# Kernel tuning notes

Measured on AMD Instinct MI355X. Metric: run time of the kernel, lower is better.

## Reference

```python
import jax, jax.numpy as jnp
import numpy as np

N = 40000          # nodes
E = 1280000        # edges (avg degree 32)
S = 64             # num_scalars
V = 16             # num_vectors
R = 32             # num_radial
CUTOFF = 10.0


def setup_inputs() -> dict:
    key = jax.random.key(0)
    ks = jax.random.split(key, 12)
    scalars = jax.random.normal(ks[0], (N, S), dtype=jnp.float32)
    vectors = jax.random.normal(ks[1], (N, V, 3), dtype=jnp.float32)
    edge_index = jax.random.randint(ks[2], (2, E), 0, N, dtype=jnp.int64)
    edge_vec = jax.random.normal(ks[3], (E, 3), dtype=jnp.float32)
    # radial_net: Linear(R,R) -> SiLU -> Linear(R, S + 2V)
    W1 = jax.random.normal(ks[4], (R, R), dtype=jnp.float32) * 0.1
    b1 = jnp.zeros((R,), dtype=jnp.float32)
    W2 = jax.random.normal(ks[5], (R, S + 2 * V), dtype=jnp.float32) * 0.1
    b2 = jnp.zeros((S + 2 * V,), dtype=jnp.float32)
    # attention: Linear(2S+R, S) -> SiLU -> Linear(S, 1)
    Wa1 = jax.random.normal(ks[6], (2 * S + R, S), dtype=jnp.float32) * 0.1
    ba1 = jnp.zeros((S,), dtype=jnp.float32)
    Wa2 = jax.random.normal(ks[7], (S, 1), dtype=jnp.float32) * 0.1
    ba2 = jnp.zeros((1,), dtype=jnp.float32)
    return dict(scalars=scalars, vectors=vectors, edge_vec=edge_vec,
                W1=W1, b1=b1, W2=W2, b2=b2,
                Wa1=Wa1, ba1=ba1, Wa2=Wa2, ba2=ba2,
                edge_index=edge_index)


def reference(scalars, vectors, edge_vec, W1, b1, W2, b2, Wa1, ba1, Wa2, ba2, edge_index):
    src = edge_index[0]  # j (source)
    dst = edge_index[1]  # i (target / aggregation index)

    d = jnp.linalg.norm(edge_vec, axis=-1)                 # [E]
    d_safe = jnp.clip(d[:, None], 1e-8, None)              # [E,1]

    # Bessel radial basis with cosine cutoff
    freqs = (jnp.arange(1, R + 1, dtype=jnp.float32) * np.pi / CUTOFF)
    bessel = jnp.sin(freqs * d[:, None]) / d_safe          # [E,R]
    cut = 0.5 * (jnp.cos(np.pi * d[:, None] / CUTOFF) + 1.0)
    cut = cut * (d[:, None] < CUTOFF).astype(jnp.float32)
    rbf = bessel * cut                                     # [E,R]

    # spherical harmonics (lmax=1); vector already normalized, sh = [1, y, z, x]
    unit = edge_vec / d_safe                               # [E,3]
    sh_weight = jnp.stack([unit[:, 1], unit[:, 2], unit[:, 0]], axis=-1)  # [E,3]

    # radial filter MLP
    filters = jax.nn.silu(rbf @ W1 + b1) @ W2 + b2         # [E, S+2V]
    scalar_filter = filters[:, :S]
    vector_filter = filters[:, S:S + V]
    vector_gate = filters[:, S + V:]

    s_i = scalars[dst]                                     # [E,S]
    s_j = scalars[src]                                     # [E,S]
    v_j = vectors[src]                                     # [E,V,3]

    scalar_message = s_j * scalar_filter                   # [E,S]
    vector_message = (v_j * vector_filter[:, :, None]
                      + vector_gate[:, :, None] * sh_weight[:, None, :])  # [E,V,3]

    att_in = jnp.concatenate([s_i, s_j, rbf], axis=-1)     # [E, 2S+R]
    att = jax.nn.sigmoid(jax.nn.silu(att_in @ Wa1 + ba1) @ Wa2 + ba2)  # [E,1]

    scalar_message = att * scalar_message
    vector_message = att[:, :, None] * vector_message

    scalar_aggr = jax.ops.segment_sum(scalar_message, dst, num_segments=N)
    vector_aggr = jax.ops.segment_sum(vector_message, dst, num_segments=N)

    return scalars + scalar_aggr, vectors + vector_aggr
```

## Files before the change

kernel.cpp:

```cpp
#include <hip/hip_runtime.h>

static constexpr int N_ = 40000;
static constexpr int E_ = 1280000;
static constexpr int NS = N_ * 64;
static constexpr int NV = N_ * 48;

typedef _Float16 half2_t __attribute__((ext_vector_type(2)));
typedef _Float16 half8_t __attribute__((ext_vector_type(8)));
typedef float float4_t __attribute__((ext_vector_type(4)));
typedef unsigned int uint;

__device__ __forceinline__ float silu_f(float x) { return __fdividef(x, 1.f + __expf(-x)); }
__device__ __forceinline__ int rfl(int x) { return __builtin_amdgcn_readfirstlane(x); }

static constexpr int PATT_BLOCKS = 512;
__global__ __launch_bounds__(256) void k_patt(
    const float* __restrict__ scalars, const float* __restrict__ Wa1,
    const float* __restrict__ ba1,
    _Float16* __restrict__ P1h, _Float16* __restrict__ P2h)
{
    int gw   = (blockIdx.x * 256 + threadIdx.x) >> 6;
    int lane = threadIdx.x & 63;
    float w[128];
#pragma unroll
    for (int k = 0; k < 128; k++) w[k] = Wa1[k * 64 + lane];
    float bias = ba1[lane];
    for (int n = gw; n < N_; n += PATT_BLOCKS * 4) {
        float sv = scalars[(size_t)n * 64 + lane];
        float a1 = bias, a2 = 0.f;
#pragma unroll
        for (int k = 0; k < 64; k++) {
            float sk = __shfl(sv, k, 64);
            a1 = fmaf(sk, w[k], a1);
            a2 = fmaf(sk, w[64 + k], a2);
        }
        P1h[(size_t)n * 64 + lane] = (_Float16)a1;
        P2h[(size_t)n * 64 + lane] = (_Float16)a2;
    }
}

__global__ void k_convp(const float* __restrict__ scalars, const float* __restrict__ vectors,
                        _Float16* __restrict__ sc16p, _Float16* __restrict__ vec16p)
{
    int t = blockIdx.x * 256 + threadIdx.x;
    if (t < N_ * 16) {
        int n = t >> 4, bl = t & 15;
        const float* srow = scalars + (size_t)n * 64;
        half2_t a, b;
        a.x = (_Float16)srow[bl];
        a.y = (_Float16)srow[16 + bl];
        b.x = (_Float16)srow[32 + bl];
        b.y = (_Float16)srow[48 + bl];
        uint2 u; u.x = __builtin_bit_cast(uint, a); u.y = __builtin_bit_cast(uint, b);
        *(uint2*)(sc16p + (size_t)n * 64 + bl * 4) = u;
    } else {
        int tt = t - N_ * 16;
        int n = tt >> 4, bl = tt & 15;
        const float* vrow = vectors + (size_t)n * 48 + bl * 3;
        half2_t a, b;
        a.x = (_Float16)vrow[0];
        a.y = (_Float16)vrow[1];
        b.x = (_Float16)vrow[2];
        b.y = (_Float16)0.f;
        uint2 u; u.x = __builtin_bit_cast(uint, a); u.y = __builtin_bit_cast(uint, b);
        *(uint2*)(vec16p + (size_t)n * 64 + bl * 4) = u;
    }
}

__global__ void k_pack(const float* __restrict__ W1, const float* __restrict__ Wa1,
                       const float* __restrict__ W2, uint* __restrict__ tbl,
                       uint* __restrict__ tbl2)
{
    int t = blockIdx.x * 256 + threadIdx.x;
    if (t < 1536) {
        int j = t >> 4, q = t & 15;
        int k0 = 2 * q, k1 = 2 * q + 1;
        float a = (j < 64) ? Wa1[(128 + k0) * 64 + j] : W1[k0 * 32 + (j - 64)];
        float b = (j < 64) ? Wa1[(128 + k1) * 64 + j] : W1[k1 * 32 + (j - 64)];
        half2_t v; v.x = (_Float16)a; v.y = (_Float16)b;
        tbl[t] = __builtin_bit_cast(uint, v);
    } else if (t < 3072) {
        int tt = t - 1536;
        int j = tt >> 4, q = tt & 15;
        half2_t v;
        v.x = (_Float16)W2[(2 * q + 0) * 96 + j];
        v.y = (_Float16)W2[(2 * q + 1) * 96 + j];
        tbl2[tt] = __builtin_bit_cast(uint, v);
    }
}

__global__ void k_rank(const int* __restrict__ eidx, int* __restrict__ cnt,
                       int* __restrict__ r)
{
    int e = blockIdx.x * 256 + threadIdx.x;
    r[e] = atomicAdd(&cnt[eidx[E_ + e]], 1);
}

__global__ void k_scan1(const int* __restrict__ cnt, int* __restrict__ row_start,
                        int* __restrict__ bsum)
{
    __shared__ int buf[1024];
    int b = blockIdx.x, tid = threadIdx.x;
    int idx = b * 1024 + tid;
    int v = (idx < N_) ? cnt[idx] : 0;
    buf[tid] = v;
    __syncthreads();
    for (int off = 1; off < 1024; off <<= 1) {
        int t = (tid >= off) ? buf[tid - off] : 0;
        __syncthreads();
        buf[tid] += t;
        __syncthreads();
    }
    if (idx < N_) row_start[idx] = buf[tid] - v;
    if (tid == 1023) bsum[b] = buf[1023];
}

__global__ void k_scan2(const int* __restrict__ bsum, int* __restrict__ boff)
{
    if (threadIdx.x == 0) {
        int s = 0;
        for (int b = 0; b < 40; b++) { boff[b] = s; s += bsum[b]; }
    }
}

__global__ void k_scan3(const int* __restrict__ boff, int* __restrict__ row_start)
{
    int idx = blockIdx.x * 1024 + threadIdx.x;
    if (idx < N_) row_start[idx] += boff[blockIdx.x];
    if (idx == N_) row_start[N_] = E_;
}

__global__ void k_place(const int* __restrict__ eidx, const int* __restrict__ row_start,
                        const int* __restrict__ r, int* __restrict__ perm)
{
    int e = blockIdx.x * 256 + threadIdx.x;
    int dst = eidx[E_ + e];
    perm[row_start[dst] + r[e]] = e;
}

__global__ __launch_bounds__(256, 3) void k_edges_sorted(
    const float* __restrict__ edge_vec, const int* __restrict__ eidx,
    const int* __restrict__ perm,
    const _Float16* __restrict__ P1h, const _Float16* __restrict__ P2h,
    const uint* __restrict__ tbl, const float* __restrict__ b1,
    const float* __restrict__ Wa2, const float* __restrict__ ba2,
    float4* __restrict__ attsh, int* __restrict__ srcbuf, uint* __restrict__ hbufp)
{
    __shared__ char lds_raw[4 * 12544];
    int tid = threadIdx.x;
    int wid = tid >> 6, lane = tid & 63;
    char* wbase = lds_raw + wid * 12544;
    int bl = lane & 15, bq = lane >> 4;

    int i = blockIdx.x * 256 + tid;
    int e = perm[i];
    int src = eidx[e];
    int dst = eidx[E_ + e];

    float ev0 = edge_vec[3 * e + 0];
    float ev1 = edge_vec[3 * e + 1];
    float ev2 = edge_vec[3 * e + 2];
    float d = sqrtf(fmaf(ev0, ev0, fmaf(ev1, ev1, ev2 * ev2)));
    float inv_d = __fdividef(1.f, fmaxf(d, 1e-8f));
    float cut = (d < 10.f) ? 0.5f * (__cosf(0.31415927f * d) + 1.f) : 0.f;
    float cutd = cut * inv_d;
    float sh0 = ev1 * inv_d, sh1 = ev2 * inv_d, sh2 = ev0 * inv_d;

    float th = 0.31415927f * d;
    float scur = __sinf(th);
    float twoC = 2.f * __cosf(th);
    float sprev = 0.f;
    uint rbf2[16];
#pragma unroll
    for (int q = 0; q < 16; q++) {
        float r0 = scur * cutd;
        float snext = fmaf(twoC, scur, -sprev);
        sprev = scur; scur = snext;
        float r1 = scur * cutd;
        snext = fmaf(twoC, scur, -sprev);
        sprev = scur; scur = snext;
        half2_t v; v.x = (_Float16)r0; v.y = (_Float16)r1;
        rbf2[q] = __builtin_bit_cast(uint, v);
    }
    {
        uint4* rw = (uint4*)(wbase + lane * 64);
        rw[0] = make_uint4(rbf2[0], rbf2[1], rbf2[2], rbf2[3]);
        rw[1] = make_uint4(rbf2[4], rbf2[5], rbf2[6], rbf2[7]);
        rw[2] = make_uint4(rbf2[8], rbf2[9], rbf2[10], rbf2[11]);
        rw[3] = make_uint4(rbf2[12], rbf2[13], rbf2[14], rbf2[15]);
    }
    uint4 bfr[6];
#pragma unroll
    for (int u = 0; u < 6; u++)
        bfr[u] = *(const uint4*)(tbl + (u * 16 + bl) * 16 + bq * 4);

    uint4 afr[4];
#pragma unroll
    for (int t = 0; t < 4; t++)
        afr[t] = *(const uint4*)(wbase + (t * 16 + bl) * 64 + bq * 16);

    _Float16* gtile = (_Float16*)wbase;
#pragma unroll
    for (int t = 0; t < 4; t++) {
        half8_t av = __builtin_bit_cast(half8_t, afr[t]);
        int eb = t * 16 + bq * 4;
#pragma unroll
        for (int u = 0; u < 6; u++) {
            float4_t dd = __builtin_amdgcn_mfma_f32_16x16x32_f16(
                av, __builtin_bit_cast(half8_t, bfr[u]), (float4_t)(0.f), 0, 0, 0);
            int col = u * 16 + bl;
            gtile[(eb + 0) * 98 + col] = (_Float16)dd[0];
            gtile[(eb + 1) * 98 + col] = (_Float16)dd[1];
            gtile[(eb + 2) * 98 + col] = (_Float16)dd[2];
            gtile[(eb + 3) * 98 + col] = (_Float16)dd[3];
        }
    }
    const uint* grow = (const uint*)(wbase + (size_t)lane * 196);

    const uint2* p1h = (const uint2*)(P1h + (size_t)dst * 64);
    const uint2* p2h = (const uint2*)(P2h + (size_t)src * 64);
    float logit = ba2[0];
#pragma unroll
    for (int q = 0; q < 16; q++) {
        uint2 ua = p1h[q];
        uint2 ub = p2h[q];
        half2_t s01 = __builtin_bit_cast(half2_t, ua.x) + __builtin_bit_cast(half2_t, ub.x)
                    + __builtin_bit_cast(half2_t, grow[2 * q + 0]);
        half2_t s23 = __builtin_bit_cast(half2_t, ua.y) + __builtin_bit_cast(half2_t, ub.y)
                    + __builtin_bit_cast(half2_t, grow[2 * q + 1]);
        logit = fmaf(silu_f((float)s01.x), Wa2[4 * q + 0], logit);
        logit = fmaf(silu_f((float)s01.y), Wa2[4 * q + 1], logit);
        logit = fmaf(silu_f((float)s23.x), Wa2[4 * q + 2], logit);
        logit = fmaf(silu_f((float)s23.y), Wa2[4 * q + 3], logit);
    }
    float att = __fdividef(1.f, 1.f + __expf(-logit));

    uint hp[16];
#pragma unroll
    for (int q = 0; q < 16; q++) {
        half2_t gg = __builtin_bit_cast(half2_t, grow[32 + q]);
        half2_t v;
        v.x = (_Float16)silu_f((float)gg.x + b1[2 * q + 0]);
        v.y = (_Float16)silu_f((float)gg.y + b1[2 * q + 1]);
        hp[q] = __builtin_bit_cast(uint, v);
    }
    uint4* hrow4 = (uint4*)(hbufp + (size_t)i * 16);
#pragma unroll
    for (int q = 0; q < 4; q++)
        hrow4[q] = make_uint4(hp[4 * q + 0], hp[4 * q + 1], hp[4 * q + 2], hp[4 * q + 3]);
    attsh[i] = make_float4(att, sh0, sh1, sh2);
    srcbuf[i] = src;
}

__global__ __launch_bounds__(256, 4) void k_gather_mfma(
    const float* __restrict__ scalars, const float* __restrict__ vectors,
    const _Float16* __restrict__ sc16p, const _Float16* __restrict__ vec16p,
    const float* __restrict__ b2,
    const int* __restrict__ row_start,
    const float4* __restrict__ attsh, const int* __restrict__ srcbuf,
    const uint* __restrict__ hbuf, const uint* __restrict__ tbl2,
    float* __restrict__ out)
{
    int wid  = threadIdx.x >> 6;
    int lane = threadIdx.x & 63;
    int n    = blockIdx.x * 4 + wid;
    int bl = lane & 15, bq = lane >> 4;
    int rs = rfl(row_start[n]);
    int re = rfl(row_start[n + 1]);

    uint4 bfr2[6];
#pragma unroll
    for (int u = 0; u < 6; u++)
        bfr2[u] = *(const uint4*)(tbl2 + (u * 16 + bl) * 16 + bq * 4);

    float b2s[4];
#pragma unroll
    for (int u = 0; u < 4; u++) b2s[u] = b2[u * 16 + bl];
    float bvf = b2[64 + bl], bvg = b2[80 + bl];

    float accS0 = 0.f, accS1 = 0.f, accS2 = 0.f, accS3 = 0.f;
    float accV0 = 0.f, accV1 = 0.f, accV2 = 0.f;

    for (int i0 = rs; i0 < re; i0 += 16) {
        uint4 av4 = make_uint4(0u, 0u, 0u, 0u);
        if (i0 + bl < re)
            av4 = *(const uint4*)(hbuf + (size_t)(i0 + bl) * 16 + bq * 4);
        half8_t av = __builtin_bit_cast(half8_t, av4);

        float4_t d0 = __builtin_amdgcn_mfma_f32_16x16x32_f16(av, __builtin_bit_cast(half8_t, bfr2[0]), (float4_t)(0.f), 0, 0, 0);
        float4_t d1 = __builtin_amdgcn_mfma_f32_16x16x32_f16(av, __builtin_bit_cast(half8_t, bfr2[1]), (float4_t)(0.f), 0, 0, 0);
        float4_t d2 = __builtin_amdgcn_mfma_f32_16x16x32_f16(av, __builtin_bit_cast(half8_t, bfr2[2]), (float4_t)(0.f), 0, 0, 0);
        float4_t d3 = __builtin_amdgcn_mfma_f32_16x16x32_f16(av, __builtin_bit_cast(half8_t, bfr2[3]), (float4_t)(0.f), 0, 0, 0);
        float4_t d4 = __builtin_amdgcn_mfma_f32_16x16x32_f16(av, __builtin_bit_cast(half8_t, bfr2[4]), (float4_t)(0.f), 0, 0, 0);
        float4_t d5 = __builtin_amdgcn_mfma_f32_16x16x32_f16(av, __builtin_bit_cast(half8_t, bfr2[5]), (float4_t)(0.f), 0, 0, 0);

#pragma unroll
        for (int r = 0; r < 4; r++) {
            int slot = i0 + bq * 4 + r;
            int ok = (slot < re);
            int cs = ok ? slot : (re - 1);
            float4 as = attsh[cs];
            float att = ok ? as.x : 0.f;
            int src = srcbuf[cs];
            uint2 su = *(const uint2*)(sc16p + (size_t)src * 64 + bl * 4);
            uint2 vu = *(const uint2*)(vec16p + (size_t)src * 64 + bl * 4);
            half2_t s01 = __builtin_bit_cast(half2_t, su.x);
            half2_t s23 = __builtin_bit_cast(half2_t, su.y);
            half2_t v01 = __builtin_bit_cast(half2_t, vu.x);
            half2_t v23 = __builtin_bit_cast(half2_t, vu.y);
            accS0 = fmaf(att * (float)s01.x, d0[r] + b2s[0], accS0);
            accS1 = fmaf(att * (float)s01.y, d1[r] + b2s[1], accS1);
            accS2 = fmaf(att * (float)s23.x, d2[r] + b2s[2], accS2);
            accS3 = fmaf(att * (float)s23.y, d3[r] + b2s[3], accS3);
            float vf = d4[r] + bvf;
            float vg = d5[r] + bvg;
            accV0 = fmaf(att, fmaf((float)v01.x, vf, vg * as.y), accV0);
            accV1 = fmaf(att, fmaf((float)v01.y, vf, vg * as.z), accV1);
            accV2 = fmaf(att, fmaf((float)v23.x, vf, vg * as.w), accV2);
        }
    }

    accS0 += __shfl_xor(accS0, 16, 64); accS0 += __shfl_xor(accS0, 32, 64);
    accS1 += __shfl_xor(accS1, 16, 64); accS1 += __shfl_xor(accS1, 32, 64);
    accS2 += __shfl_xor(accS2, 16, 64); accS2 += __shfl_xor(accS2, 32, 64);
    accS3 += __shfl_xor(accS3, 16, 64); accS3 += __shfl_xor(accS3, 32, 64);
    accV0 += __shfl_xor(accV0, 16, 64); accV0 += __shfl_xor(accV0, 32, 64);
    accV1 += __shfl_xor(accV1, 16, 64); accV1 += __shfl_xor(accV1, 32, 64);
    accV2 += __shfl_xor(accV2, 16, 64); accV2 += __shfl_xor(accV2, 32, 64);

    if (bq == 0) {
        size_t o = (size_t)n * 64 + bl;
        out[o +  0] = scalars[o +  0] + accS0;
        out[o + 16] = scalars[o + 16] + accS1;
        out[o + 32] = scalars[o + 32] + accS2;
        out[o + 48] = scalars[o + 48] + accS3;
        size_t ov = (size_t)n * 48 + 3 * bl;
        out[NS + ov + 0] = vectors[ov + 0] + accV0;
        out[NS + ov + 1] = vectors[ov + 1] + accV1;
        out[NS + ov + 2] = vectors[ov + 2] + accV2;
    }
}

extern "C" void kernel_launch(void* const* d_in, const int* in_sizes, int n_in,
                              void* d_out, int out_size, void* d_ws, size_t ws_size,
                              hipStream_t stream)
{
    const float* scalars  = (const float*)d_in[0];
    const float* vectors  = (const float*)d_in[1];
    const float* edge_vec = (const float*)d_in[2];
    const float* W1  = (const float*)d_in[3];
    const float* b1  = (const float*)d_in[4];
    const float* W2  = (const float*)d_in[5];
    const float* b2  = (const float*)d_in[6];
    const float* Wa1 = (const float*)d_in[7];
    const float* ba1 = (const float*)d_in[8];
    const float* Wa2 = (const float*)d_in[9];
    const float* ba2 = (const float*)d_in[10];
    const int* eidx  = (const int*)d_in[11];

    char* wsb = (char*)d_ws;
    float4* attsh = (float4*)wsb;
    float*  P1    = (float*)(wsb + (size_t)E_ * 16);
    float*  P2    = P1 + NS;
    float*  hbuf  = P2 + NS;
    int* cnt       = (int*)(hbuf + (size_t)32 * E_);
    int* bsum      = cnt + N_;
    int* boff      = bsum + 64;
    int* row_start = cnt + 2 * N_;
    int* perm      = row_start + N_ + 1;
    int* srcbuf    = perm + E_;
    int*  rnk  = (int*)hbuf;
    uint* tbl  = (uint*)hbuf + (size_t)16 * E_;
    uint* tbl2 = tbl + 1536;
    _Float16* P1h  = (_Float16*)(tbl2 + 1536);
    _Float16* P2h  = P1h + NS;
    _Float16* sc16p = P2h + NS;
    _Float16* vec16p = (_Float16*)P1;

    hipMemsetAsync(cnt, 0, (size_t)N_ * sizeof(int), stream);
    k_pack<<<12, 256, 0, stream>>>(W1, Wa1, W2, tbl, tbl2);
    k_rank<<<5000, 256, 0, stream>>>(eidx, cnt, rnk);
    k_scan1<<<40, 1024, 0, stream>>>(cnt, row_start, bsum);
    k_scan2<<<1, 64, 0, stream>>>(bsum, boff);
    k_scan3<<<40, 1024, 0, stream>>>(boff, row_start);
    k_place<<<5000, 256, 0, stream>>>(eidx, row_start, rnk, perm);
    k_patt<<<PATT_BLOCKS, 256, 0, stream>>>(scalars, Wa1, ba1, P1h, P2h);
    k_convp<<<5000, 256, 0, stream>>>(scalars, vectors, sc16p, vec16p);
    k_edges_sorted<<<5000, 256, 0, stream>>>(edge_vec, eidx, perm, P1h, P2h,
                                             tbl, b1, Wa2, ba2,
                                             attsh, srcbuf, (uint*)hbuf);
    k_gather_mfma<<<10000, 256, 0, stream>>>(scalars, vectors, sc16p, vec16p, b2, row_start,
                                             attsh, srcbuf, (const uint*)hbuf, tbl2,
                                             (float*)d_out);
}
```

Measured before the change: 392.7 us.

## Scatter edge data into sorted order at placement, fold small kernels

The placement kernel now writes edge vectors (padded to float4), source and destination indices directly into dst-sorted slots. The edge kernel can then read them contiguously instead of doing an indirect perm lookup followed by random gathers. The weight-packing kernel is merged into the conversion kernel as extra blocks, and the two-step block-offset scan is collapsed into one kernel where each block sums its preceding block totals. This removes two launches and the random reads in the heavy edge kernel, at the cost of a random scatter of more data during placement.

After: 404.6 us. 1.03x slower.

```diff
diff --git a/kernel.cpp b/kernel.cpp
--- a/kernel.cpp
+++ b/kernel.cpp
@@ -40,8 +40,30 @@
 }
 
 __global__ void k_convp(const float* __restrict__ scalars, const float* __restrict__ vectors,
-                        _Float16* __restrict__ sc16p, _Float16* __restrict__ vec16p)
-{
+                        _Float16* __restrict__ sc16p, _Float16* __restrict__ vec16p,
+                        const float* __restrict__ W1, const float* __restrict__ Wa1,
+                        const float* __restrict__ W2, uint* __restrict__ tbl,
+                        uint* __restrict__ tbl2)
+{
+    if (blockIdx.x >= 5000) {
+        int t = (blockIdx.x - 5000) * 256 + threadIdx.x;
+        if (t < 1536) {
+            int j = t >> 4, q = t & 15;
+            int k0 = 2 * q, k1 = 2 * q + 1;
+            float a = (j < 64) ? Wa1[(128 + k0) * 64 + j] : W1[k0 * 32 + (j - 64)];
+            float b = (j < 64) ? Wa1[(128 + k1) * 64 + j] : W1[k1 * 32 + (j - 64)];
+            half2_t v; v.x = (_Float16)a; v.y = (_Float16)b;
+            tbl[t] = __builtin_bit_cast(uint, v);
+        } else if (t < 3072) {
+            int tt = t - 1536;
+            int j = tt >> 4, q = tt & 15;
+            half2_t v;
+            v.x = (_Float16)W2[(2 * q + 0) * 96 + j];
+            v.y = (_Float16)W2[(2 * q + 1) * 96 + j];
+            tbl2[tt] = __builtin_bit_cast(uint, v);
+        }
+        return;
+    }
     int t = blockIdx.x * 256 + threadIdx.x;
     if (t < N_ * 16) {
         int n = t >> 4, bl = t & 15;
@@ -67,28 +89,6 @@
     }
 }
 
-__global__ void k_pack(const float* __restrict__ W1, const float* __restrict__ Wa1,
-                       const float* __restrict__ W2, uint* __restrict__ tbl,
-                       uint* __restrict__ tbl2)
-{
-    int t = blockIdx.x * 256 + threadIdx.x;
-    if (t < 1536) {
-        int j = t >> 4, q = t & 15;
-        int k0 = 2 * q, k1 = 2 * q + 1;
-        float a = (j < 64) ? Wa1[(128 + k0) * 64 + j] : W1[k0 * 32 + (j - 64)];
-        float b = (j < 64) ? Wa1[(128 + k1) * 64 + j] : W1[k1 * 32 + (j - 64)];
-        half2_t v; v.x = (_Float16)a; v.y = (_Float16)b;
-        tbl[t] = __builtin_bit_cast(uint, v);
-    } else if (t < 3072) {
-        int tt = t - 1536;
-        int j = tt >> 4, q = tt & 15;
-        half2_t v;
-        v.x = (_Float16)W2[(2 * q + 0) * 96 + j];
-        v.y = (_Float16)W2[(2 * q + 1) * 96 + j];
-        tbl2[tt] = __builtin_bit_cast(uint, v);
-    }
-}
-
 __global__ void k_rank(const int* __restrict__ eidx, int* __restrict__ cnt,
                        int* __restrict__ r)
 {
@@ -115,36 +115,41 @@
     if (tid == 1023) bsum[b] = buf[1023];
 }
 
-__global__ void k_scan2(const int* __restrict__ bsum, int* __restrict__ boff)
-{
+__global__ void k_scan3(const int* __restrict__ bsum, int* __restrict__ row_start)
+{
+    __shared__ int boffs;
     if (threadIdx.x == 0) {
         int s = 0;
-        for (int b = 0; b < 40; b++) { boff[b] = s; s += bsum[b]; }
-    }
-}
-
-__global__ void k_scan3(const int* __restrict__ boff, int* __restrict__ row_start)
-{
+        for (int b = 0; b < (int)blockIdx.x; b++) s += bsum[b];
+        boffs = s;
+    }
+    __syncthreads();
     int idx = blockIdx.x * 1024 + threadIdx.x;
-    if (idx < N_) row_start[idx] += boff[blockIdx.x];
+    if (idx < N_) row_start[idx] += boffs;
     if (idx == N_) row_start[N_] = E_;
 }
 
-__global__ void k_place(const int* __restrict__ eidx, const int* __restrict__ row_start,
-                        const int* __restrict__ r, int* __restrict__ perm)
+__global__ void k_place2(const int* __restrict__ eidx, const float* __restrict__ edge_vec,
+                         const int* __restrict__ row_start, const int* __restrict__ r,
+                         float4* __restrict__ evs, int* __restrict__ srcs,
+                         int* __restrict__ dsts)
 {
     int e = blockIdx.x * 256 + threadIdx.x;
+    int src = eidx[e];
     int dst = eidx[E_ + e];
-    perm[row_start[dst] + r[e]] = e;
+    int slot = row_start[dst] + r[e];
+    evs[slot] = make_float4(edge_vec[3 * e + 0], edge_vec[3 * e + 1], edge_vec[3 * e + 2], 0.f);
+    srcs[slot] = src;
+    dsts[slot] = dst;
 }
 
 __global__ __launch_bounds__(256, 3) void k_edges_sorted(
-    const float* __restrict__ edge_vec, const int* __restrict__ eidx,
-    const int* __restrict__ perm,
+    const float4* __restrict__ evs, const int* __restrict__ srcs,
+    const int* __restrict__ dsts,
     const _Float16* __restrict__ P1h, const _Float16* __restrict__ P2h,
     const uint* __restrict__ tbl, const float* __restrict__ b1,
     const float* __restrict__ Wa2, const float* __restrict__ ba2,
-    float4* __restrict__ attsh, int* __restrict__ srcbuf, uint* __restrict__ hbufp)
+    float4* __restrict__ attsh, uint* __restrict__ hbufp)
 {
     __shared__ char lds_raw[4 * 12544];
     int tid = threadIdx.x;
@@ -153,13 +158,11 @@
     int bl = lane & 15, bq = lane >> 4;
 
     int i = blockIdx.x * 256 + tid;
-    int e = perm[i];
-    int src = eidx[e];
-    int dst = eidx[E_ + e];
-
-    float ev0 = edge_vec[3 * e + 0];
-    float ev1 = edge_vec[3 * e + 1];
-    float ev2 = edge_vec[3 * e + 2];
+    float4 ev4 = evs[i];
+    int src = srcs[i];
+    int dst = dsts[i];
+
+    float ev0 = ev4.x, ev1 = ev4.y, ev2 = ev4.z;
     float d = sqrtf(fmaf(ev0, ev0, fmaf(ev1, ev1, ev2 * ev2)));
     float inv_d = __fdividef(1.f, fmaxf(d, 1e-8f));
     float cut = (d < 10.f) ? 0.5f * (__cosf(0.31415927f * d) + 1.f) : 0.f;
@@ -249,7 +252,6 @@
     for (int q = 0; q < 4; q++)
         hrow4[q] = make_uint4(hp[4 * q + 0], hp[4 * q + 1], hp[4 * q + 2], hp[4 * q + 3]);
     attsh[i] = make_float4(att, sh0, sh1, sh2);
-    srcbuf[i] = src;
 }
 
 __global__ __launch_bounds__(256, 4) void k_gather_mfma(
@@ -376,19 +378,19 @@
     _Float16* P2h  = P1h + NS;
     _Float16* sc16p = P2h + NS;
     _Float16* vec16p = (_Float16*)P1;
+    float4* evs = (float4*)(sc16p + NS);
+    int* dsts   = (int*)(evs + E_);
 
     hipMemsetAsync(cnt, 0, (size_t)N_ * sizeof(int), stream);
-    k_pack<<<12, 256, 0, stream>>>(W1, Wa1, W2, tbl, tbl2);
     k_rank<<<5000, 256, 0, stream>>>(eidx, cnt, rnk);
     k_scan1<<<40, 1024, 0, stream>>>(cnt, row_start, bsum);
-    k_scan2<<<1, 64, 0, stream>>>(bsum, boff);
-    k_scan3<<<40, 1024, 0, stream>>>(boff, row_start);
-    k_place<<<5000, 256, 0, stream>>>(eidx, row_start, rnk, perm);
+    k_scan3<<<40, 1024, 0, stream>>>(bsum, row_start);
+    k_place2<<<5000, 256, 0, stream>>>(eidx, edge_vec, row_start, rnk, evs, srcbuf, dsts);
     k_patt<<<PATT_BLOCKS, 256, 0, stream>>>(scalars, Wa1, ba1, P1h, P2h);
-    k_convp<<<5000, 256, 0, stream>>>(scalars, vectors, sc16p, vec16p);
-    k_edges_sorted<<<5000, 256, 0, stream>>>(edge_vec, eidx, perm, P1h, P2h,
+    k_convp<<<5012, 256, 0, stream>>>(scalars, vectors, sc16p, vec16p, W1, Wa1, W2, tbl, tbl2);
+    k_edges_sorted<<<5000, 256, 0, stream>>>(evs, srcbuf, dsts, P1h, P2h,
                                              tbl, b1, Wa2, ba2,
-                                             attsh, srcbuf, (uint*)hbuf);
+                                             attsh, (uint*)hbuf);
     k_gather_mfma<<<10000, 256, 0, stream>>>(scalars, vectors, sc16p, vec16p, b2, row_start,
                                              attsh, srcbuf, (const uint*)hbuf, tbl2,
                                              (float*)d_out);
```
